# Performance work log

Hardware: AMD Instinct MI355X
Metric: run time of the kernel (lower is better)

Reference implementation:

```python
import jax, jax.numpy as jnp
import numpy as np
import math

B, T, D = 1, 4096, 1024
H = 16
HD = D // H  # 64


def _rotate_half(x):
    d = x.shape[-1] // 2
    return jnp.concatenate([-x[..., d:], x[..., :d]], axis=-1)


def setup_inputs() -> dict:
    key = jax.random.key(0)
    k1, k2, k3 = jax.random.split(key, 3)
    x = jax.random.normal(k1, (B, T, D), dtype=jnp.float32)
    # Linear weights stored as (in, out) so forward is x @ W
    w_qkv = jax.random.normal(k2, (D, 3 * D), dtype=jnp.float32) * (1.0 / math.sqrt(D))
    w_proj = jax.random.normal(k3, (D, D), dtype=jnp.float32) * (1.0 / math.sqrt(D))
    return {"x": x, "w_qkv": w_qkv, "w_proj": w_proj}


def reference(x, w_qkv, w_proj):
    b, t, c = x.shape
    qkv = x @ w_qkv  # [b,t,3c]
    q, k, v = jnp.split(qkv, 3, axis=-1)
    # [b,h,t,hd]
    q = q.reshape(b, t, H, HD).transpose(0, 2, 1, 3)
    k = k.reshape(b, t, H, HD).transpose(0, 2, 1, 3)
    v = v.reshape(b, t, H, HD).transpose(0, 2, 1, 3)

    # RoPE (rotate_half style)
    inv_freq = 1.0 / (10000.0 ** (jnp.arange(0, HD, 2, dtype=jnp.float32) / HD))
    pos = jnp.arange(t, dtype=jnp.float32)
    freqs = jnp.outer(pos, inv_freq)            # [t, hd/2]
    cos = jnp.concatenate([jnp.cos(freqs), jnp.cos(freqs)], axis=-1)[None, None]  # [1,1,t,hd]
    sin = jnp.concatenate([jnp.sin(freqs), jnp.sin(freqs)], axis=-1)[None, None]
    q = q * cos + _rotate_half(q) * sin
    k = k * cos + _rotate_half(k) * sin

    att = jnp.einsum('bhqd,bhkd->bhqk', q, k) / math.sqrt(HD)  # [b,h,t,t]
    causal = jnp.tril(jnp.ones((t, t), dtype=bool))
    att = jnp.where(causal, att, -jnp.inf)
    att = jax.nn.softmax(att, axis=-1)
    # dropout is identity in eval mode
    y = jnp.einsum('bhqk,bhkd->bhqd', att, v)
    y = y.transpose(0, 2, 1, 3).reshape(b, t, c)
    return y @ w_proj
```

## Files before the change

kernel.cpp:

```cpp
#include <hip/hip_runtime.h>
#include <hip/hip_fp16.h>
#include <math.h>

#define TT 4096
#define DD 1024
#define NH 16
#define HD 64

typedef __attribute__((ext_vector_type(8))) _Float16 half8v;
typedef __attribute__((ext_vector_type(4))) _Float16 half4v;
typedef __attribute__((ext_vector_type(4))) float f32x4;

#define GLDS16(g, l)                                                        \
    __builtin_amdgcn_global_load_lds(                                       \
        (const __attribute__((address_space(1))) void*)(g),                 \
        (__attribute__((address_space(3))) void*)(l), 16, 0, 0)

__global__ __launch_bounds__(256) void cast_x(const float* __restrict__ X,
                                              _Float16* __restrict__ Xh)
{
    const int i = (blockIdx.x * 256 + threadIdx.x) * 8;
    float4 a = *(const float4*)&X[i];
    float4 b = *(const float4*)&X[i + 4];
    half8v o = {(_Float16)a.x, (_Float16)a.y, (_Float16)a.z, (_Float16)a.w,
                (_Float16)b.x, (_Float16)b.y, (_Float16)b.z, (_Float16)b.w};
    *(half8v*)&Xh[i] = o;
}

__global__ __launch_bounds__(256) void transpose_cast(
    const float* __restrict__ W, _Float16* __restrict__ WT, int K, int N)
{
    __shared__ float tile[64][65];
    const int t = threadIdx.x;
    const int k0 = blockIdx.y * 64, n0 = blockIdx.x * 64;
    const int c = (t & 15) * 4, r = t >> 4;
#pragma unroll
    for (int i = 0; i < 4; i++) {
        float4 v = *(const float4*)&W[(size_t)(k0 + r + 16 * i) * N + n0 + c];
        tile[r + 16 * i][c + 0] = v.x;
        tile[r + 16 * i][c + 1] = v.y;
        tile[r + 16 * i][c + 2] = v.z;
        tile[r + 16 * i][c + 3] = v.w;
    }
    __syncthreads();
#pragma unroll
    for (int i = 0; i < 4; i++) {
        const int n = r + 16 * i;
        half4v o;
        o[0] = (_Float16)tile[c + 0][n];
        o[1] = (_Float16)tile[c + 1][n];
        o[2] = (_Float16)tile[c + 2][n];
        o[3] = (_Float16)tile[c + 3][n];
        *(half4v*)&WT[(size_t)(n0 + n) * K + k0 + c] = o;
    }
}

template <int MODE>
__global__ __launch_bounds__(256) void gemm_h(
    const _Float16* __restrict__ A, const _Float16* __restrict__ Bt,
    float* __restrict__ C0, _Float16* __restrict__ Q,
    _Float16* __restrict__ Kk, _Float16* __restrict__ V,
    int M, int N, int K)
{
    __shared__ _Float16 As[128 * 32];
    __shared__ _Float16 Bs[128 * 32];
    const int tid  = threadIdx.x;
    const int wave = tid >> 6;
    const int lane = tid & 63;
    const int quad = lane >> 4;
    const int n16  = lane & 15;
    const int n0 = blockIdx.x * 128;
    const int m0 = blockIdx.y * 128;
    const int wr = (wave & 1) * 64;
    const int wc = (wave >> 1) * 64;

    f32x4 acc[4][4];
#pragma unroll
    for (int i = 0; i < 4; i++)
#pragma unroll
        for (int j = 0; j < 4; j++) acc[i][j] = (f32x4){0.f, 0.f, 0.f, 0.f};

    const int srow = tid >> 2;
    const int scol = (tid & 3) * 8;
    const _Float16* Ag = A + (size_t)(m0 + srow) * K + scol;
    const _Float16* Bg = Bt + (size_t)(n0 + srow) * K + scol;
    _Float16* AsW = As + (size_t)wave * 512;
    _Float16* BsW = Bs + (size_t)wave * 512;

    for (int k0 = 0; k0 < K; k0 += 32) {
        __syncthreads();
        GLDS16(Ag + k0, AsW);
        GLDS16(Ag + (size_t)64 * K + k0, AsW + 2048);
        GLDS16(Bg + k0, BsW);
        GLDS16(Bg + (size_t)64 * K + k0, BsW + 2048);
        __syncthreads();

        half8v aF[4], bF[4];
#pragma unroll
        for (int i = 0; i < 4; i++)
            aF[i] = *(const half8v*)&As[(size_t)(wr + i * 16 + n16) * 32 + quad * 8];
#pragma unroll
        for (int j = 0; j < 4; j++)
            bF[j] = *(const half8v*)&Bs[(size_t)(wc + j * 16 + n16) * 32 + quad * 8];
#pragma unroll
        for (int i = 0; i < 4; i++)
#pragma unroll
            for (int j = 0; j < 4; j++)
                acc[i][j] = __builtin_amdgcn_mfma_f32_16x16x32_f16(
                    aF[i], bF[j], acc[i][j], 0, 0, 0);
    }

#pragma unroll
    for (int i = 0; i < 4; i++) {
#pragma unroll
        for (int j = 0; j < 4; j++) {
#pragma unroll
            for (int r = 0; r < 4; r++) {
                const int m = m0 + wr + i * 16 + quad * 4 + r;
                const int n = n0 + wc + j * 16 + n16;
                const float val = acc[i][j][r];
                if (MODE == 0) {
                    C0[(size_t)m * N + n] = val;
                } else {
                    const int which = n >> 10;
                    const int col = n & 1023;
                    const int h = col >> 6, d = col & 63;
                    const size_t off = ((size_t)h * TT + m) * HD + d;
                    if (which == 0) Q[off] = (_Float16)val;
                    else if (which == 1) Kk[off] = (_Float16)val;
                    else V[off] = (_Float16)val;
                }
            }
        }
    }
}

__global__ __launch_bounds__(256) void rope_h(_Float16* __restrict__ Q,
                                              _Float16* __restrict__ Kb)
{
    const int idx = blockIdx.x * 256 + threadIdx.x;
    const int i = idx & 31;
    const int t = (idx >> 5) & (TT - 1);
    const int h = idx >> 17;
    if (h >= NH) return;

    const float inv = expf(-(float)i * (logf(10000.0f) / 32.0f));
    const float f = (float)t * inv;
    const float c = cosf(f), s = sinf(f);
    const size_t base = ((size_t)h * TT + t) * HD + i;
    const float QS = 0.125f * 1.44269504f;

    float q1 = (float)Q[base], q2 = (float)Q[base + 32];
    Q[base]      = (_Float16)((q1 * c - q2 * s) * QS);
    Q[base + 32] = (_Float16)((q2 * c + q1 * s) * QS);
    float k1 = (float)Kb[base], k2 = (float)Kb[base + 32];
    Kb[base]      = (_Float16)(k1 * c - k2 * s);
    Kb[base + 32] = (_Float16)(k2 * c + k1 * s);
}

__global__ __launch_bounds__(256) void transpose_v(
    const _Float16* __restrict__ V, _Float16* __restrict__ Vp)
{
    __shared__ _Float16 tile[256][72];
    const int h = blockIdx.y;
    const int t0 = blockIdx.x * 256;
    const int tid = threadIdx.x;
    const _Float16* Vg = V + (size_t)h * TT * HD;

#pragma unroll
    for (int i = 0; i < 4; i++) {
        const int chunk = tid + 256 * i;
        const int row = chunk >> 2, c = (chunk & 3) * 16;
        half8v v0 = *(const half8v*)(Vg + (size_t)(t0 + row) * HD + c);
        half8v v1 = *(const half8v*)(Vg + (size_t)(t0 + row) * HD + c + 8);
        *(half8v*)&tile[row][c] = v0;
        *(half8v*)&tile[row][c + 8] = v1;
    }
    __syncthreads();

    _Float16* Vo = Vp + ((size_t)h * (TT / 32) + (t0 >> 5)) * 64 * 32;
#pragma unroll
    for (int i = 0; i < 8; i++) {
        const int item = tid + 256 * i;
        const int cc = (item & 3) * 8;
        const int d = (item >> 2) & 63;
        const int kbl = item >> 8;
        half8v o;
#pragma unroll
        for (int e = 0; e < 8; e++) {
            const int cp = cc + e;
            const int key = (cp >> 1) + 16 * (cp & 1);
            o[e] = tile[kbl * 32 + key][d];
        }
        *(half8v*)(Vo + ((size_t)kbl * 64 + d) * 32 + cc) = o;
    }
}

__global__ __launch_bounds__(256) void zero_acc(float4* __restrict__ O4,
                                                float4* __restrict__ L4)
{
    const int i = blockIdx.x * 256 + threadIdx.x;
    const float4 z = {0.f, 0.f, 0.f, 0.f};
    O4[i] = z;
    if (i < 16384) L4[i] = z;
}

__global__ __launch_bounds__(256) void attn_kernel(
    const _Float16* __restrict__ Qh, const _Float16* __restrict__ Kh,
    const _Float16* __restrict__ Vp, _Float16* __restrict__ Oacc,
    float* __restrict__ Lacc)
{
    __shared__ _Float16 Ks[2][32][32];
    __shared__ _Float16 Vs[64][32];
    __shared__ _Float16 Ps[4][32][40];

    const int tid  = threadIdx.x;
    const int wave = tid >> 6;
    const int lane = tid & 63;
    const int quad = lane >> 4;
    const int n16  = lane & 15;
    const int h  = blockIdx.z;
    const int qt = 31 - blockIdx.y;
    const int s  = blockIdx.x;
    const int nT = 4 * qt + 4;
    const int nS = (qt + 8) >> 3;
    if (s >= nS) return;
    const int t_beg = s * nT / nS;
    const int t_end = (s + 1) * nT / nS;

    const int q0 = qt * 128;
    const int rowbase = q0 + wave * 32;

    const _Float16* Qg = Qh + (size_t)h * TT * HD;
    const _Float16* Kg = Kh + (size_t)h * TT * HD;
    const _Float16* Vg = Vp + (size_t)h * (TT / 32) * 64 * 32;

    half8v aQ[2][2];
#pragma unroll
    for (int g = 0; g < 2; g++) {
        const int row = rowbase + g * 16 + n16;
#pragma unroll
        for (int c = 0; c < 2; c++)
            aQ[g][c] = *(const half8v*)(Qg + (size_t)row * HD + c * 32 + quad * 8);
    }

    f32x4 O[2][4];
#pragma unroll
    for (int g = 0; g < 2; g++)
#pragma unroll
        for (int d = 0; d < 4; d++) O[g][d] = (f32x4){0.f, 0.f, 0.f, 0.f};
    float l[2][4] = {{0.f, 0.f, 0.f, 0.f}, {0.f, 0.f, 0.f, 0.f}};

    const int kc = tid >> 7, kj = (tid >> 2) & 31, ks = tid & 3;
    const _Float16* kSrc = Kg + (size_t)kj * HD + kc * 32 + ks * 8;
    const _Float16* vSrc = Vg + (size_t)tid * 8;
    _Float16* ksBase = &Ks[0][0][0] + (size_t)wave * 512;
    _Float16* vsBase = &Vs[0][0] + (size_t)wave * 512;

    for (int it = t_beg; it < t_end; ++it) {
        const int j0 = it * 32;
        __syncthreads();
        GLDS16(kSrc + (size_t)j0 * HD, ksBase);
        GLDS16(vSrc + (size_t)it * 2048, vsBase);
        __syncthreads();

        if (j0 <= rowbase + 31) {
            const bool needMask = (j0 + 31 > rowbase);

            f32x4 S[2][2];
#pragma unroll
            for (int g = 0; g < 2; g++)
#pragma unroll
                for (int st = 0; st < 2; st++) {
                    S[g][st] = (f32x4){0.f, 0.f, 0.f, 0.f};
#pragma unroll
                    for (int c = 0; c < 2; c++) {
                        half8v bK = *(const half8v*)&Ks[c][st * 16 + n16][quad * 8];
                        S[g][st] = __builtin_amdgcn_mfma_f32_16x16x32_f16(
                            aQ[g][c], bK, S[g][st], 0, 0, 0);
                    }
                }

#pragma unroll
            for (int g = 0; g < 2; g++)
#pragma unroll
                for (int r = 0; r < 4; r++) {
                    const int row = rowbase + g * 16 + quad * 4 + r;
                    float x0 = S[g][0][r];
                    float x1 = S[g][1][r];
                    if (needMask) {
                        x0 = (j0 + n16      <= row) ? x0 : -1e30f;
                        x1 = (j0 + 16 + n16 <= row) ? x1 : -1e30f;
                    }
                    const float p0 = __builtin_amdgcn_exp2f(x0);
                    const float p1 = __builtin_amdgcn_exp2f(x1);
                    l[g][r] += p0 + p1;
                    *(__half2*)&Ps[wave][g * 16 + quad * 4 + r][2 * n16] =
                        __floats2half2_rn(p0, p1);
                }

            half8v bV[4];
#pragma unroll
            for (int d = 0; d < 4; d++)
                bV[d] = *(const half8v*)&Vs[d * 16 + n16][quad * 8];
#pragma unroll
            for (int g = 0; g < 2; g++) {
                half8v aP = *(const half8v*)&Ps[wave][g * 16 + n16][quad * 8];
#pragma unroll
                for (int d = 0; d < 4; d++)
                    O[g][d] = __builtin_amdgcn_mfma_f32_16x16x32_f16(
                        aP, bV[d], O[g][d], 0, 0, 0);
            }
        }
    }

#pragma unroll
    for (int g = 0; g < 2; g++)
#pragma unroll
        for (int r = 0; r < 4; r++) {
            float sl = l[g][r];
            sl += __shfl_xor(sl, 1);
            sl += __shfl_xor(sl, 2);
            sl += __shfl_xor(sl, 4);
            sl += __shfl_xor(sl, 8);
            const int row = rowbase + g * 16 + quad * 4 + r;
            if (n16 == 0)
                unsafeAtomicAdd(&Lacc[h * TT + row], sl);
#pragma unroll
            for (int d = 0; d < 4; d++) {
                float v = O[g][d][r];
                float vn = __shfl_xor(v, 1);
                if ((lane & 1) == 0) {
                    __half2* dst = (__half2*)(Oacc +
                        ((size_t)h * TT + row) * HD + d * 16 + n16);
                    unsafeAtomicAdd(dst, __floats2half2_rn(v, vn));
                }
            }
        }
}

__global__ __launch_bounds__(256) void finalize(
    const _Float16* __restrict__ Oacc, const float* __restrict__ Lacc,
    _Float16* __restrict__ Y)
{
    const int gid = blockIdx.x * 256 + threadIdx.x;
    const int h = gid >> 15;
    const int rem = gid & 32767;
    const int t = rem >> 3;
    const int c = rem & 7;
    const float inv = 1.0f / Lacc[h * TT + t];
    half8v o = *(const half8v*)(Oacc + ((size_t)h * TT + t) * HD + c * 8);
    half8v y;
#pragma unroll
    for (int e = 0; e < 8; e++) y[e] = (_Float16)((float)o[e] * inv);
    *(half8v*)(Y + (size_t)t * DD + h * HD + c * 8) = y;
}

extern "C" void kernel_launch(void* const* d_in, const int* in_sizes, int n_in,
                              void* d_out, int out_size, void* d_ws, size_t ws_size,
                              hipStream_t stream)
{
    const float* x      = (const float*)d_in[0];
    const float* w_qkv  = (const float*)d_in[1];
    const float* w_proj = (const float*)d_in[2];
    float* out = (float*)d_out;

    char* ws = (char*)d_ws;
    const size_t MB = 1u << 20;
    _Float16* xh   = (_Float16*)(ws);
    _Float16* WqT  = (_Float16*)(ws + 8 * MB);
    _Float16* WpT  = (_Float16*)(ws + 14 * MB);
    _Float16* Qh   = (_Float16*)(ws + 16 * MB);
    _Float16* Kh   = (_Float16*)(ws + 24 * MB);
    _Float16* Vh   = (_Float16*)(ws + 32 * MB);
    _Float16* Vp   = (_Float16*)(ws + 40 * MB);
    _Float16* Yh   = (_Float16*)(ws + 48 * MB);
    _Float16* Oacc = (_Float16*)(ws + 56 * MB);
    float*    Lacc = (float*)(ws + 65 * MB);

    dim3 blk(256);

    cast_x<<<(TT * DD) / (256 * 8), blk, 0, stream>>>(x, xh);
    transpose_cast<<<dim3(3072 / 64, DD / 64), blk, 0, stream>>>(w_qkv, WqT, DD, 3 * DD);
    transpose_cast<<<dim3(DD / 64, DD / 64), blk, 0, stream>>>(w_proj, WpT, DD, DD);

    gemm_h<1><<<dim3(3072 / 128, TT / 128), blk, 0, stream>>>(
        xh, WqT, nullptr, Qh, Kh, Vh, TT, 3 * DD, DD);

    rope_h<<<(NH * TT * 32) / 256, blk, 0, stream>>>(Qh, Kh);
    transpose_v<<<dim3(TT / 256, NH), blk, 0, stream>>>(Vh, Vp);
    zero_acc<<<2048, blk, 0, stream>>>((float4*)Oacc, (float4*)Lacc);

    attn_kernel<<<dim3(4, 32, NH), blk, 0, stream>>>(Qh, Kh, Vp, Oacc, Lacc);

    finalize<<<2048, blk, 0, stream>>>(Oacc, Lacc, Yh);

    gemm_h<0><<<dim3(DD / 128, TT / 128), blk, 0, stream>>>(
        Yh, WpT, out, nullptr, nullptr, nullptr, TT, DD, DD);
}
```

Measured before the change: 281.3 us.

## Fuse RoPE and V permutation into QKV GEMM epilogue; load K/V directly in attention

```diff
diff --git a/kernel.cpp b/kernel.cpp
--- a/kernel.cpp
+++ b/kernel.cpp
@@ -110,89 +110,59 @@
                     aF[i], bF[j], acc[i][j], 0, 0, 0);
     }
 
-#pragma unroll
-    for (int i = 0; i < 4; i++) {
-#pragma unroll
-        for (int j = 0; j < 4; j++) {
-#pragma unroll
-            for (int r = 0; r < 4; r++) {
-                const int m = m0 + wr + i * 16 + quad * 4 + r;
-                const int n = n0 + wc + j * 16 + n16;
-                const float val = acc[i][j][r];
-                if (MODE == 0) {
-                    C0[(size_t)m * N + n] = val;
-                } else {
-                    const int which = n >> 10;
-                    const int col = n & 1023;
-                    const int h = col >> 6, d = col & 63;
-                    const size_t off = ((size_t)h * TT + m) * HD + d;
-                    if (which == 0) Q[off] = (_Float16)val;
-                    else if (which == 1) Kk[off] = (_Float16)val;
-                    else V[off] = (_Float16)val;
+    if (MODE == 0) {
+#pragma unroll
+        for (int i = 0; i < 4; i++)
+#pragma unroll
+            for (int j = 0; j < 4; j++)
+#pragma unroll
+                for (int r = 0; r < 4; r++) {
+                    const int m = m0 + wr + i * 16 + quad * 4 + r;
+                    const int n = n0 + wc + j * 16 + n16;
+                    C0[(size_t)m * N + n] = acc[i][j][r];
+                }
+    } else {
+        const int ncol0 = n0 + wc;
+        const int which = ncol0 >> 10;
+        const int h = (ncol0 & 1023) >> 6;
+        if (which < 2) {
+            _Float16* dst = (which == 0) ? Q : Kk;
+            const float sc = (which == 0) ? 0.125f * 1.44269504f : 1.0f;
+            const float K2 = 0.4152410118609203f;
+#pragma unroll
+            for (int jlo = 0; jlo < 2; jlo++) {
+                const int d = jlo * 16 + n16;
+                const float invf = exp2f(-(float)d * K2);
+#pragma unroll
+                for (int i = 0; i < 4; i++) {
+#pragma unroll
+                    for (int r = 0; r < 4; r++) {
+                        const int t = m0 + wr + i * 16 + quad * 4 + r;
+                        const float f = (float)t * invf;
+                        float sn, cs;
+                        __sincosf(f, &sn, &cs);
+                        const float lo = acc[i][jlo][r];
+                        const float hi = acc[i][jlo + 2][r];
+                        const size_t off = ((size_t)h * TT + t) * HD + d;
+                        dst[off]      = (_Float16)((lo * cs - hi * sn) * sc);
+                        dst[off + 32] = (_Float16)((hi * cs + lo * sn) * sc);
+                    }
                 }
             }
+        } else {
+#pragma unroll
+            for (int i = 0; i < 4; i++)
+#pragma unroll
+                for (int j = 0; j < 4; j++)
+#pragma unroll
+                    for (int r = 0; r < 4; r++) {
+                        const int t = m0 + wr + i * 16 + quad * 4 + r;
+                        const int d = j * 16 + n16;
+                        const int cp = 2 * (t & 15) + ((t >> 4) & 1);
+                        V[(((size_t)h * (TT / 32) + (t >> 5)) * 64 + d) * 32 + cp] =
+                            (_Float16)acc[i][j][r];
+                    }
         }
-    }
-}
-
-__global__ __launch_bounds__(256) void rope_h(_Float16* __restrict__ Q,
-                                              _Float16* __restrict__ Kb)
-{
-    const int idx = blockIdx.x * 256 + threadIdx.x;
-    const int i = idx & 31;
-    const int t = (idx >> 5) & (TT - 1);
-    const int h = idx >> 17;
-    if (h >= NH) return;
-
-    const float inv = expf(-(float)i * (logf(10000.0f) / 32.0f));
-    const float f = (float)t * inv;
-    const float c = cosf(f), s = sinf(f);
-    const size_t base = ((size_t)h * TT + t) * HD + i;
-    const float QS = 0.125f * 1.44269504f;
-
-    float q1 = (float)Q[base], q2 = (float)Q[base + 32];
-    Q[base]      = (_Float16)((q1 * c - q2 * s) * QS);
-    Q[base + 32] = (_Float16)((q2 * c + q1 * s) * QS);
-    float k1 = (float)Kb[base], k2 = (float)Kb[base + 32];
-    Kb[base]      = (_Float16)(k1 * c - k2 * s);
-    Kb[base + 32] = (_Float16)(k2 * c + k1 * s);
-}
-
-__global__ __launch_bounds__(256) void transpose_v(
-    const _Float16* __restrict__ V, _Float16* __restrict__ Vp)
-{
-    __shared__ _Float16 tile[256][72];
-    const int h = blockIdx.y;
-    const int t0 = blockIdx.x * 256;
-    const int tid = threadIdx.x;
-    const _Float16* Vg = V + (size_t)h * TT * HD;
-
-#pragma unroll
-    for (int i = 0; i < 4; i++) {
-        const int chunk = tid + 256 * i;
-        const int row = chunk >> 2, c = (chunk & 3) * 16;
-        half8v v0 = *(const half8v*)(Vg + (size_t)(t0 + row) * HD + c);
-        half8v v1 = *(const half8v*)(Vg + (size_t)(t0 + row) * HD + c + 8);
-        *(half8v*)&tile[row][c] = v0;
-        *(half8v*)&tile[row][c + 8] = v1;
-    }
-    __syncthreads();
-
-    _Float16* Vo = Vp + ((size_t)h * (TT / 32) + (t0 >> 5)) * 64 * 32;
-#pragma unroll
-    for (int i = 0; i < 8; i++) {
-        const int item = tid + 256 * i;
-        const int cc = (item & 3) * 8;
-        const int d = (item >> 2) & 63;
-        const int kbl = item >> 8;
-        half8v o;
-#pragma unroll
-        for (int e = 0; e < 8; e++) {
-            const int cp = cc + e;
-            const int key = (cp >> 1) + 16 * (cp & 1);
-            o[e] = tile[kbl * 32 + key][d];
-        }
-        *(half8v*)(Vo + ((size_t)kbl * 64 + d) * 32 + cc) = o;
     }
 }
 
@@ -210,8 +180,6 @@
     const _Float16* __restrict__ Vp, _Float16* __restrict__ Oacc,
     float* __restrict__ Lacc)
 {
-    __shared__ _Float16 Ks[2][32][32];
-    __shared__ _Float16 Vs[64][32];
     __shared__ _Float16 Ps[4][32][40];
 
     const int tid  = threadIdx.x;
@@ -233,7 +201,7 @@
 
     const _Float16* Qg = Qh + (size_t)h * TT * HD;
     const _Float16* Kg = Kh + (size_t)h * TT * HD;
-    const _Float16* Vg = Vp + (size_t)h * (TT / 32) * 64 * 32;
+    const _Float16* Vg = Vp + (size_t)h * (TT / 32) * 2048;
 
     half8v aQ[2][2];
 #pragma unroll
@@ -251,66 +219,61 @@
         for (int d = 0; d < 4; d++) O[g][d] = (f32x4){0.f, 0.f, 0.f, 0.f};
     float l[2][4] = {{0.f, 0.f, 0.f, 0.f}, {0.f, 0.f, 0.f, 0.f}};
 
-    const int kc = tid >> 7, kj = (tid >> 2) & 31, ks = tid & 3;
-    const _Float16* kSrc = Kg + (size_t)kj * HD + kc * 32 + ks * 8;
-    const _Float16* vSrc = Vg + (size_t)tid * 8;
-    _Float16* ksBase = &Ks[0][0][0] + (size_t)wave * 512;
-    _Float16* vsBase = &Vs[0][0] + (size_t)wave * 512;
-
     for (int it = t_beg; it < t_end; ++it) {
         const int j0 = it * 32;
-        __syncthreads();
-        GLDS16(kSrc + (size_t)j0 * HD, ksBase);
-        GLDS16(vSrc + (size_t)it * 2048, vsBase);
-        __syncthreads();
-
-        if (j0 <= rowbase + 31) {
-            const bool needMask = (j0 + 31 > rowbase);
-
-            f32x4 S[2][2];
-#pragma unroll
-            for (int g = 0; g < 2; g++)
-#pragma unroll
-                for (int st = 0; st < 2; st++) {
-                    S[g][st] = (f32x4){0.f, 0.f, 0.f, 0.f};
-#pragma unroll
-                    for (int c = 0; c < 2; c++) {
-                        half8v bK = *(const half8v*)&Ks[c][st * 16 + n16][quad * 8];
-                        S[g][st] = __builtin_amdgcn_mfma_f32_16x16x32_f16(
-                            aQ[g][c], bK, S[g][st], 0, 0, 0);
-                    }
+        if (j0 > rowbase + 31) break;
+        const bool needMask = (j0 + 31 > rowbase);
+
+        half8v bK[2][2];
+#pragma unroll
+        for (int st = 0; st < 2; st++)
+#pragma unroll
+            for (int c = 0; c < 2; c++)
+                bK[c][st] = *(const half8v*)(
+                    Kg + (size_t)(j0 + st * 16 + n16) * HD + c * 32 + quad * 8);
+        half8v bV[4];
+#pragma unroll
+        for (int d = 0; d < 4; d++)
+            bV[d] = *(const half8v*)(
+                Vg + (size_t)it * 2048 + (d * 16 + n16) * 32 + quad * 8);
+
+        f32x4 S[2][2];
+#pragma unroll
+        for (int g = 0; g < 2; g++)
+#pragma unroll
+            for (int st = 0; st < 2; st++) {
+                S[g][st] = (f32x4){0.f, 0.f, 0.f, 0.f};
+#pragma unroll
+                for (int c = 0; c < 2; c++)
+                    S[g][st] = __builtin_amdgcn_mfma_f32_16x16x32_f16(
+                        aQ[g][c], bK[c][st], S[g][st], 0, 0, 0);
+            }
+
+#pragma unroll
+        for (int g = 0; g < 2; g++)
+#pragma unroll
+            for (int r = 0; r < 4; r++) {
+                const int row = rowbase + g * 16 + quad * 4 + r;
+                float x0 = S[g][0][r];
+                float x1 = S[g][1][r];
+                if (needMask) {
+                    x0 = (j0 + n16      <= row) ? x0 : -1e30f;
+                    x1 = (j0 + 16 + n16 <= row) ? x1 : -1e30f;
                 }
-
-#pragma unroll
-            for (int g = 0; g < 2; g++)
-#pragma unroll
-                for (int r = 0; r < 4; r++) {
-                    const int row = rowbase + g * 16 + quad * 4 + r;
-                    float x0 = S[g][0][r];
-                    float x1 = S[g][1][r];
-                    if (needMask) {
-                        x0 = (j0 + n16      <= row) ? x0 : -1e30f;
-                        x1 = (j0 + 16 + n16 <= row) ? x1 : -1e30f;
-                    }
-                    const float p0 = __builtin_amdgcn_exp2f(x0);
-                    const float p1 = __builtin_amdgcn_exp2f(x1);
-                    l[g][r] += p0 + p1;
-                    *(__half2*)&Ps[wave][g * 16 + quad * 4 + r][2 * n16] =
-                        __floats2half2_rn(p0, p1);
-                }
-
-            half8v bV[4];
+                const float p0 = __builtin_amdgcn_exp2f(x0);
+                const float p1 = __builtin_amdgcn_exp2f(x1);
+                l[g][r] += p0 + p1;
+                *(__half2*)&Ps[wave][g * 16 + quad * 4 + r][2 * n16] =
+                    __floats2half2_rn(p0, p1);
+            }
+
+#pragma unroll
+        for (int g = 0; g < 2; g++) {
+            half8v aP = *(const half8v*)&Ps[wave][g * 16 + n16][quad * 8];
 #pragma unroll
             for (int d = 0; d < 4; d++)
-                bV[d] = *(const half8v*)&Vs[d * 16 + n16][quad * 8];
-#pragma unroll
-            for (int g = 0; g < 2; g++) {
-                half8v aP = *(const half8v*)&Ps[wave][g * 16 + n16][quad * 8];
-#pragma unroll
-                for (int d = 0; d < 4; d++)
-                    O[g][d] = __builtin_amdgcn_mfma_f32_16x16x32_f16(
-                        aP, bV[d], O[g][d], 0, 0, 0);
-            }
+                O[g][d] = __builtin_amdgcn_mfma_f32_16x16x32_f16(
+                    aP, bV[d], O[g][d], 0, 0, 0);
         }
     }
 
@@ -372,11 +335,10 @@
     _Float16* WpT  = (_Float16*)(ws + 14 * MB);
     _Float16* Qh   = (_Float16*)(ws + 16 * MB);
     _Float16* Kh   = (_Float16*)(ws + 24 * MB);
-    _Float16* Vh   = (_Float16*)(ws + 32 * MB);
-    _Float16* Vp   = (_Float16*)(ws + 40 * MB);
-    _Float16* Yh   = (_Float16*)(ws + 48 * MB);
-    _Float16* Oacc = (_Float16*)(ws + 56 * MB);
-    float*    Lacc = (float*)(ws + 65 * MB);
+    _Float16* Vp   = (_Float16*)(ws + 32 * MB);
+    _Float16* Yh   = (_Float16*)(ws + 40 * MB);
+    _Float16* Oacc = (_Float16*)(ws + 48 * MB);
+    float*    Lacc = (float*)(ws + 57 * MB);
 
     dim3 blk(256);
 
@@ -385,10 +347,8 @@
     transpose_cast<<<dim3(DD / 64, DD / 64), blk, 0, stream>>>(w_proj, WpT, DD, DD);
 
     gemm_h<1><<<dim3(3072 / 128, TT / 128), blk, 0, stream>>>(
-        xh, WqT, nullptr, Qh, Kh, Vh, TT, 3 * DD, DD);
-
-    rope_h<<<(NH * TT * 32) / 256, blk, 0, stream>>>(Qh, Kh);
-    transpose_v<<<dim3(TT / 256, NH), blk, 0, stream>>>(Vh, Vp);
+        xh, WqT, nullptr, Qh, Kh, Vp, TT, 3 * DD, DD);
+
     zero_acc<<<2048, blk, 0, stream>>>((float4*)Oacc, (float4*)Lacc);
 
     attn_kernel<<<dim3(4, 32, NH), blk, 0, stream>>>(Qh, Kh, Vp, Oacc, Lacc);
```

Result: slower. 352.3 us (+25.2%).
